# Kernel optimization log

Hardware: AMD Instinct MI355X
Metric: run time of the kernel (lower is better)

## Reference

```python
import jax, jax.numpy as jnp
import numpy as np
from jax import lax

B, D, E, H, W = 256, 64, 16, 64, 64
PROJ, FC, NA = 512, 1024, 2

def _conv(x, w, pad):
    # x: [N,C,H,W], w: [O,I,kh,kw]
    return lax.conv_general_dilated(x, w, (1, 1), [(pad, pad), (pad, pad)],
                                    dimension_numbers=('NCHW', 'OIHW', 'NCHW'))

def _maxpool2(x):
    return lax.reduce_window(x, -jnp.inf, lax.max, (1, 1, 2, 2), (1, 1, 2, 2), 'VALID')

def _sample_conv(x, w, b):
    # per-sample conv with its own gathered expert weights: x [D,h,w], w [D,D,3,3]
    y = lax.conv_general_dilated(x[None], w, (1, 1), [(1, 1), (1, 1)],
                                 dimension_numbers=('NCHW', 'OIHW', 'NCHW'))[0]
    return y + b[:, None, None]

_expert_conv = jax.vmap(_sample_conv)  # batch of samples, each with its own kernel

def setup_inputs() -> dict:
    key = jax.random.key(0)
    ks = jax.random.split(key, 12)
    s = 0.05
    return {
        'image': jax.random.normal(ks[0], (B, 3, H, W), jnp.float32),
        'question': jax.random.randint(ks[1], (B, 8), 0, E),
        'stem_w0': jax.random.normal(ks[2], (D, 3, 3, 3), jnp.float32) * s,
        'stem_b0': jnp.zeros((D,), jnp.float32),
        'stem_w': jax.random.normal(ks[3], (3, D, D, 3, 3), jnp.float32) * s,
        'stem_b': jnp.zeros((3, D), jnp.float32),
        'exp_w1': jax.random.normal(ks[4], (E, D, D, 3, 3), jnp.float32) * s,
        'exp_b1': jnp.zeros((E, D), jnp.float32),
        'exp_w2': jax.random.normal(ks[5], (E, D, D, 3, 3), jnp.float32) * s,
        'exp_b2': jnp.zeros((E, D), jnp.float32),
        'proj_w': jax.random.normal(ks[6], (PROJ, D, 1, 1), jnp.float32) * s,
        'proj_b': jnp.zeros((PROJ,), jnp.float32),
        'fc1_w': jax.random.normal(ks[7], (FC, PROJ * 8 * 8), jnp.float32) * 0.01,
        'fc1_b': jnp.zeros((FC,), jnp.float32),
        'fc2_w': jax.random.normal(ks[8], (NA, FC), jnp.float32) * 0.01,
        'fc2_b': jnp.zeros((NA,), jnp.float32),
    }

def reference(image, question, stem_w0, stem_b0, stem_w, stem_b,
              exp_w1, exp_b1, exp_w2, exp_b2,
              proj_w, proj_b, fc1_w, fc1_b, fc2_w, fc2_b):
    # --- stem: 4 conv3x3 + ReLU, maxpool after layers 0 and 2 (64->32->16) ---
    h = jax.nn.relu(_conv(image, stem_w0, 1) + stem_b0[None, :, None, None])
    h = _maxpool2(h)
    h = jax.nn.relu(_conv(h, stem_w[0], 1) + stem_b[0][None, :, None, None])
    h = jax.nn.relu(_conv(h, stem_w[1], 1) + stem_b[1][None, :, None, None])
    h = _maxpool2(h)
    h = jax.nn.relu(_conv(h, stem_w[2], 1) + stem_b[2][None, :, None, None])
    # --- chain1 routing: cols (lhs=4, rel=5, rhs=7) each pick a ResidualBlock expert ---
    for col in (4, 5, 7):
        idx = question[:, col]                       # [B] expert ids
        w1, b1 = exp_w1[idx], exp_b1[idx]            # gather per-sample kernels
        w2, b2 = exp_w2[idx], exp_b2[idx]
        mid = jax.nn.relu(_expert_conv(h, w1, b1))   # conv1 + ReLU
        out = _expert_conv(mid, w2, b2)              # conv2 (no BN)
        h = jax.nn.relu(h + out)                     # residual + ReLU
    # --- classifier: 1x1 proj + ReLU, maxpool2, flatten, fc, fc ---
    c = jax.nn.relu(_conv(h, proj_w, 0) + proj_b[None, :, None, None])  # [B,512,16,16]
    c = _maxpool2(c)                                                     # [B,512,8,8]
    c = c.reshape(c.shape[0], -1)                                        # [B,32768]
    c = jax.nn.relu(c @ fc1_w.T + fc1_b)
    return c @ fc2_w.T + fc2_b                                           # [B,2]
```

## Files before the change

### kernel.cpp

```cpp
#include <hip/hip_runtime.h>
#include <cstddef>


typedef _Float16 half8 __attribute__((ext_vector_type(8)));
typedef _Float16 half4_t __attribute__((ext_vector_type(4)));
typedef float f32x4 __attribute__((ext_vector_type(4)));

#define LO_SCALE 2048.0f
#define LO_INV (1.0f / 2048.0f)

__global__ void transw_k(const float* __restrict__ src, float* __restrict__ dst,
                         int O, int I, int K, int total) {
    int id = blockIdx.x * 256 + threadIdx.x;
    if (id >= total) return;
    int OIK = O * I * K;
    int n = id / OIK, rem = id % OIK;
    int o = rem / (I * K), r2 = rem % (I * K);
    int i = r2 / K, k = r2 % K;
    dst[(size_t)n * OIK + (i * K + k) * O + o] = src[id];
}

__global__ void wxform_k(const float* __restrict__ src, _Float16* __restrict__ dst,
                         int nlayers) {
    int id = blockIdx.x * 256 + threadIdx.x;
    if (id >= nlayers * 36864) return;
    int layer = id / 36864, idx = id % 36864;
    int j = idx & 7, l = (idx >> 3) & 63, nt = (idx >> 9) & 3;
    int icc = (idx >> 11) & 1, tap = idx >> 12;
    int kl = (l >> 4) * 8 + j, ic = icc * 32 + kl, oc = nt * 16 + (l & 15);
    float v = src[(size_t)layer * 36864 + (oc * 64 + ic) * 9 + tap];
    _Float16 hi = (_Float16)v;
    _Float16 lo = (_Float16)((v - (float)hi) * LO_SCALE);
    dst[(size_t)layer * 73728 + idx] = hi;
    dst[(size_t)layer * 73728 + 36864 + idx] = lo;
}

__global__ __launch_bounds__(256)
void conv1_k(const float* __restrict__ img, const float* __restrict__ w0t,
             const float* __restrict__ b0, float* __restrict__ out) {
    int b = blockIdx.x, tile = blockIdx.y;
    int typ = (tile >> 1) * 16, txp = (tile & 1) * 16;
    int cy0 = typ * 2, cx0 = txp * 2;
    __shared__ float lds[3][34][34];
    const float* imb = img + (size_t)b * 3 * 64 * 64;
    for (int i = threadIdx.x; i < 3 * 34 * 34; i += 256) {
        int c = i / 1156, rem = i % 1156, r = rem / 34, cc = rem % 34;
        int gy = cy0 - 1 + r, gx = cx0 - 1 + cc;
        float v = 0.f;
        if (gy >= 0 && gy < 64 && gx >= 0 && gx < 64) v = imb[(c * 64 + gy) * 64 + gx];
        lds[c][r][cc] = v;
    }
    __syncthreads();
    int pyl = threadIdx.x >> 4, pxl = threadIdx.x & 15;
    float win[3][4][4];
#pragma unroll
    for (int c = 0; c < 3; ++c)
#pragma unroll
        for (int wy = 0; wy < 4; ++wy)
#pragma unroll
            for (int wx = 0; wx < 4; ++wx)
                win[c][wy][wx] = lds[c][2 * pyl + wy][2 * pxl + wx];
    int py = typ + pyl, px = txp + pxl;
    for (int oc = 0; oc < 64; ++oc) {
        float a00 = 0, a01 = 0, a10 = 0, a11 = 0;
#pragma unroll
        for (int c = 0; c < 3; ++c)
#pragma unroll
            for (int ky = 0; ky < 3; ++ky)
#pragma unroll
                for (int kx = 0; kx < 3; ++kx) {
                    float w = w0t[(c * 9 + ky * 3 + kx) * 64 + oc];
                    a00 = fmaf(win[c][0 + ky][0 + kx], w, a00);
                    a01 = fmaf(win[c][0 + ky][1 + kx], w, a01);
                    a10 = fmaf(win[c][1 + ky][0 + kx], w, a10);
                    a11 = fmaf(win[c][1 + ky][1 + kx], w, a11);
                }
        float bv = b0[oc];
        float v = fmaxf(fmaxf(a00 + bv, 0.f), fmaxf(a01 + bv, 0.f));
        v = fmaxf(v, fmaxf(fmaxf(a10 + bv, 0.f), fmaxf(a11 + bv, 0.f)));
        out[(((size_t)b * 32 + py) * 32 + px) * 64 + oc] = v;
    }
}

template <int S, bool POOL, bool RES>
__global__ __launch_bounds__(256, 2)
void convm_k(const float* __restrict__ in, float* __restrict__ out,
             const _Float16* __restrict__ wf, const float* __restrict__ bias,
             const float* __restrict__ res, const int* __restrict__ question,
             int qcol) {
    int b = blockIdx.x, t = blockIdx.y;
    constexpr int NTX = S / 16;
    int ty0 = (t / NTX) * 8, tx0 = (t % NTX) * 16;

    __shared__ __align__(16) _Float16 lds[2 * 7200];

    int tid = threadIdx.x, lane = tid & 63, wv = tid >> 6;
    const _Float16* wb = wf;
    const float* bb = bias;
    if (question) {
        int idx = question[b * 8 + qcol];
        wb += (size_t)idx * 73728;
        bb += idx * 64;
    }
    float bv[4];
#pragma unroll
    for (int nt = 0; nt < 4; ++nt) bv[nt] = bb[nt * 16 + (lane & 15)];

    f32x4 acc1[2][4] = {};
    f32x4 acc2[2][4] = {};

    int am = lane & 15;
    int k0 = (lane >> 4) * 8;

    for (int icc = 0; icc < 2; ++icc) {
        __syncthreads();
        for (int i = tid; i < 1440; i += 256) {
            int pix = i >> 3, j4 = i & 7;
            int hy = pix / 18, hx = pix % 18;
            int gy = ty0 + hy - 1, gx = tx0 + hx - 1;
            float4 v = {0.f, 0.f, 0.f, 0.f};
            if (gy >= 0 && gy < S && gx >= 0 && gx < S)
                v = *(const float4*)&in[(((size_t)b * S + gy) * S + gx) * 64 + icc * 32 + j4 * 4];
            _Float16 h0 = (_Float16)v.x, h1 = (_Float16)v.y;
            _Float16 h2 = (_Float16)v.z, h3 = (_Float16)v.w;
            half4_t hh = {h0, h1, h2, h3};
            half4_t ll = {(_Float16)((v.x - (float)h0) * LO_SCALE),
                          (_Float16)((v.y - (float)h1) * LO_SCALE),
                          (_Float16)((v.z - (float)h2) * LO_SCALE),
                          (_Float16)((v.w - (float)h3) * LO_SCALE)};
            *(half4_t*)&lds[pix * 40 + j4 * 4] = hh;
            *(half4_t*)&lds[7200 + pix * 40 + j4 * 4] = ll;
        }
        __syncthreads();

#pragma unroll
        for (int ky = 0; ky < 3; ++ky)
#pragma unroll
            for (int kx = 0; kx < 3; ++kx) {
                int tap = ky * 3 + kx;
                const _Float16* wp = wb + (tap * 2 + icc) * 2048 + lane * 8;
                half8 bhi[4], blo[4];
#pragma unroll
                for (int nt = 0; nt < 4; ++nt) {
                    bhi[nt] = *(const half8*)(wp + nt * 512);
                    blo[nt] = *(const half8*)(wp + nt * 512 + 36864);
                }
#pragma unroll
                for (int mt = 0; mt < 2; ++mt) {
                    int MT = wv * 2 + mt;
                    int Q = MT * 4 + (am >> 2), s = am & 3;
                    int py = (Q >> 3) * 2 + (s >> 1), px = (Q & 7) * 2 + (s & 1);
                    const _Float16* ap = &lds[((py + ky) * 18 + (px + kx)) * 40 + k0];
                    half8 ahi = *(const half8*)ap;
                    half8 alo = *(const half8*)(ap + 7200);
#pragma unroll
                    for (int nt = 0; nt < 4; ++nt) {
                        acc1[mt][nt] = __builtin_amdgcn_mfma_f32_16x16x32_f16(
                            ahi, bhi[nt], acc1[mt][nt], 0, 0, 0);
                        acc2[mt][nt] = __builtin_amdgcn_mfma_f32_16x16x32_f16(
                            ahi, blo[nt], acc2[mt][nt], 0, 0, 0);
                        acc2[mt][nt] = __builtin_amdgcn_mfma_f32_16x16x32_f16(
                            alo, bhi[nt], acc2[mt][nt], 0, 0, 0);
                    }
                }
            }
    }

    int cn = lane & 15, rq = lane >> 4;
#pragma unroll
    for (int mt = 0; mt < 2; ++mt) {
        int MT = wv * 2 + mt;
        int Q = MT * 4 + rq;
        int qy = Q >> 3, qx = Q & 7;
#pragma unroll
        for (int nt = 0; nt < 4; ++nt) {
            int oc = nt * 16 + cn;
            float vals[4];
#pragma unroll
            for (int r = 0; r < 4; ++r)
                vals[r] = acc1[mt][nt][r] + acc2[mt][nt][r] * LO_INV + bv[nt];
            if (POOL) {
                float m = fmaxf(fmaxf(vals[0], vals[1]), fmaxf(vals[2], vals[3]));
                m = fmaxf(m, 0.f);
                int opy = (ty0 >> 1) + qy, opx = (tx0 >> 1) + qx;
                out[(((size_t)b * (S / 2) + opy) * (S / 2) + opx) * 64 + oc] = m;
            } else {
#pragma unroll
                for (int r = 0; r < 4; ++r) {
                    int py = qy * 2 + (r >> 1), px = qx * 2 + (r & 1);
                    size_t o = (((size_t)b * S + (ty0 + py)) * S + (tx0 + px)) * 64 + oc;
                    float v = vals[r];
                    if (RES) v += res[o];
                    out[o] = fmaxf(v, 0.f);
                }
            }
        }
    }
}

__global__ __launch_bounds__(256)
void proj_k(const float* __restrict__ in, const float* __restrict__ wt ,
            const float* __restrict__ bias, float* __restrict__ out) {
    int b = blockIdx.x;
    __shared__ float lds[16384];
    const float* inb = in + (size_t)b * 16384;
    for (int i = threadIdx.x; i < 16384; i += 256) lds[i] = inb[i];
    __syncthreads();
    int lane = threadIdx.x & 63, wv = threadIdx.x >> 6;
    int oc = (blockIdx.y * 4 + wv) * 64 + lane;
    float w[64];
#pragma unroll
    for (int ic = 0; ic < 64; ++ic) w[ic] = wt[ic * 512 + oc];
    float bvv = bias[oc];
    for (int pp = 0; pp < 64; ++pp) {
        int ppy = pp >> 3, ppx = pp & 7;
        float m = 0.f;
#pragma unroll
        for (int d = 0; d < 4; ++d) {
            int py = ppy * 2 + (d >> 1), px = ppx * 2 + (d & 1);
            const float* ap = &lds[(py * 16 + px) * 64];
            float acc = bvv;
#pragma unroll
            for (int ic = 0; ic < 64; ++ic) acc = fmaf(ap[ic], w[ic], acc);
            m = fmaxf(m, acc);
        }
        out[(size_t)b * 32768 + (size_t)oc * 64 + pp] = m;
    }
}

__global__ __launch_bounds__(256)
void fc1m_k(const float* __restrict__ A, const float* __restrict__ W,
            float* __restrict__ partial ) {
    int bid = blockIdx.x;
    int lid = (bid & 7) * 64 + (bid >> 3);
    int mt = lid & 1, nt = (lid >> 1) & 7, ks = lid >> 4;
    int m0 = mt * 128, n0 = nt * 128;
    const float* Ab = A + (size_t)m0 * 32768 + ks * 1024;
    const float* Wb = W + (size_t)n0 * 32768 + ks * 1024;

    __shared__ __align__(16) _Float16 lds[20480];
    _Float16* sa = lds;
    _Float16* sb = lds + 10240;

    int tid = threadIdx.x, lane = tid & 63, wv = tid >> 6;
    int wm = (wv & 1) * 64, wn = (wv >> 1) * 64;

    f32x4 acc1[4][4] = {};
    f32x4 acc2[4][4] = {};

    int row[4], c4[4];
#pragma unroll
    for (int p = 0; p < 4; ++p) {
        int idx = p * 256 + tid;
        row[p] = idx >> 3;
        c4[p] = (idx & 7) << 2;
    }

    float4 ra[4], rw[4];
#pragma unroll
    for (int p = 0; p < 4; ++p) {
        ra[p] = *(const float4*)&Ab[(size_t)row[p] * 32768 + c4[p]];
        rw[p] = *(const float4*)&Wb[(size_t)row[p] * 32768 + c4[p]];
    }

    for (int kt = 0; kt < 32; ++kt) {
#pragma unroll
        for (int p = 0; p < 4; ++p) {
            float4 v = ra[p];
            _Float16 h0 = (_Float16)v.x, h1 = (_Float16)v.y;
            _Float16 h2 = (_Float16)v.z, h3 = (_Float16)v.w;
            half4_t hh = {h0, h1, h2, h3};
            half4_t ll = {(_Float16)((v.x - (float)h0) * LO_SCALE),
                          (_Float16)((v.y - (float)h1) * LO_SCALE),
                          (_Float16)((v.z - (float)h2) * LO_SCALE),
                          (_Float16)((v.w - (float)h3) * LO_SCALE)};
            *(half4_t*)&sa[row[p] * 40 + c4[p]] = hh;
            *(half4_t*)&sa[5120 + row[p] * 40 + c4[p]] = ll;
            float4 u = rw[p];
            _Float16 g0 = (_Float16)u.x, g1 = (_Float16)u.y;
            _Float16 g2 = (_Float16)u.z, g3 = (_Float16)u.w;
            half4_t gh = {g0, g1, g2, g3};
            half4_t gl = {(_Float16)((u.x - (float)g0) * LO_SCALE),
                          (_Float16)((u.y - (float)g1) * LO_SCALE),
                          (_Float16)((u.z - (float)g2) * LO_SCALE),
                          (_Float16)((u.w - (float)g3) * LO_SCALE)};
            *(half4_t*)&sb[row[p] * 40 + c4[p]] = gh;
            *(half4_t*)&sb[5120 + row[p] * 40 + c4[p]] = gl;
        }
        __syncthreads();
        if (kt < 31) {
            int kb = (kt + 1) * 32;
#pragma unroll
            for (int p = 0; p < 4; ++p) {
                ra[p] = *(const float4*)&Ab[(size_t)row[p] * 32768 + kb + c4[p]];
                rw[p] = *(const float4*)&Wb[(size_t)row[p] * 32768 + kb + c4[p]];
            }
        }
        int koff = (lane >> 4) * 8;
        int fr = lane & 15;
        half8 bh[4], bl[4];
#pragma unroll
        for (int nf = 0; nf < 4; ++nf) {
            int r = wn + nf * 16 + fr;
            bh[nf] = *(const half8*)&sb[r * 40 + koff];
            bl[nf] = *(const half8*)&sb[5120 + r * 40 + koff];
        }
#pragma unroll
        for (int mf = 0; mf < 4; ++mf) {
            int r = wm + mf * 16 + fr;
            half8 ah = *(const half8*)&sa[r * 40 + koff];
            half8 al = *(const half8*)&sa[5120 + r * 40 + koff];
#pragma unroll
            for (int nf = 0; nf < 4; ++nf) {
                acc1[mf][nf] = __builtin_amdgcn_mfma_f32_16x16x32_f16(
                    ah, bh[nf], acc1[mf][nf], 0, 0, 0);
                acc2[mf][nf] = __builtin_amdgcn_mfma_f32_16x16x32_f16(
                    ah, bl[nf], acc2[mf][nf], 0, 0, 0);
                acc2[mf][nf] = __builtin_amdgcn_mfma_f32_16x16x32_f16(
                    al, bh[nf], acc2[mf][nf], 0, 0, 0);
            }
        }
        __syncthreads();
    }

    int rq = lane >> 4, cn = lane & 15;
    float* pb = partial + (size_t)ks * 262144;
#pragma unroll
    for (int mf = 0; mf < 4; ++mf)
#pragma unroll
        for (int nf = 0; nf < 4; ++nf) {
            int n = n0 + wn + nf * 16 + cn;
#pragma unroll
            for (int r = 0; r < 4; ++r) {
                int m = m0 + wm + mf * 16 + rq * 4 + r;
                pb[(size_t)m * 1024 + n] = acc1[mf][nf][r] + acc2[mf][nf][r] * LO_INV;
            }
        }
}

__global__ __launch_bounds__(256)
void fc1red_k(const float* __restrict__ partial, const float* __restrict__ b1,
              float* __restrict__ fc1o_t ) {
    int m = blockIdx.x;
    int n0 = threadIdx.x * 4;
    float4 s = {0.f, 0.f, 0.f, 0.f};
    for (int ks = 0; ks < 32; ++ks) {
        float4 v = *(const float4*)&partial[((size_t)ks * 256 + m) * 1024 + n0];
        s.x += v.x; s.y += v.y; s.z += v.z; s.w += v.w;
    }
    fc1o_t[(size_t)(n0 + 0) * 256 + m] = fmaxf(s.x + b1[n0 + 0], 0.f);
    fc1o_t[(size_t)(n0 + 1) * 256 + m] = fmaxf(s.y + b1[n0 + 1], 0.f);
    fc1o_t[(size_t)(n0 + 2) * 256 + m] = fmaxf(s.z + b1[n0 + 2], 0.f);
    fc1o_t[(size_t)(n0 + 3) * 256 + m] = fmaxf(s.w + b1[n0 + 3], 0.f);
}

__global__ __launch_bounds__(256)
void fc2a_k(const float* __restrict__ a_t, const float* __restrict__ W2,
            float* __restrict__ p2) {
    int n2 = blockIdx.x, ks = blockIdx.y;
    int m = threadIdx.x;
    float acc = 0.f;
    for (int k = ks * 256; k < ks * 256 + 256; ++k)
        acc = fmaf(a_t[(size_t)k * 256 + m], W2[n2 * 1024 + k], acc);
    p2[((size_t)n2 * 4 + ks) * 256 + m] = acc;
}

__global__ __launch_bounds__(512)
void fc2b_k(const float* __restrict__ p2, const float* __restrict__ b2,
            float* __restrict__ out) {
    int i = threadIdx.x;
    int m = i >> 1, n2 = i & 1;
    float s = b2[n2];
#pragma unroll
    for (int ks = 0; ks < 4; ++ks) s += p2[((size_t)n2 * 4 + ks) * 256 + m];
    out[m * 2 + n2] = s;
}

extern "C" void kernel_launch(void* const* d_in, const int* in_sizes, int n_in,
                              void* d_out, int out_size, void* d_ws, size_t ws_size,
                              hipStream_t stream) {
    const float* image   = (const float*)d_in[0];
    const int*   question= (const int*)d_in[1];
    const float* stem_w0 = (const float*)d_in[2];
    const float* stem_b0 = (const float*)d_in[3];
    const float* stem_w  = (const float*)d_in[4];
    const float* stem_b  = (const float*)d_in[5];
    const float* exp_w1  = (const float*)d_in[6];
    const float* exp_b1  = (const float*)d_in[7];
    const float* exp_w2  = (const float*)d_in[8];
    const float* exp_b2  = (const float*)d_in[9];
    const float* proj_w  = (const float*)d_in[10];
    const float* proj_b  = (const float*)d_in[11];
    const float* fc1_w   = (const float*)d_in[12];
    const float* fc1_b   = (const float*)d_in[13];
    const float* fc2_w   = (const float*)d_in[14];
    const float* fc2_b   = (const float*)d_in[15];
    (void)in_sizes; (void)n_in; (void)out_size; (void)ws_size;

    float* ws = (float*)d_ws;
    const size_t A = 16777216, P2N = 4194304;
    float* p1    = ws;
    float* h2    = ws + A;
    float* p2    = ws + 2 * A;
    float* wtr   = ws + 2 * A + P2N;
    float* w0t   = wtr;
    float* projt = wtr + 1728;
    float* pfc2  = wtr + 1728 + 32768;
    _Float16* f16b = (_Float16*)(wtr + 36544);
    _Float16* stemtF = f16b;
    _Float16* e1tF   = f16b + 3 * 73728;
    _Float16* e2tF   = e1tF + 16 * 73728;
    float* hA    = ws;
    float* hB    = ws + P2N;
    float* hC    = ws + 2 * P2N;
    float* pool3 = h2;
    float* fc1o  = h2 + 8388608;
    float* fc1p  = ws;

    transw_k<<<(1728 + 255) / 256, 256, 0, stream>>>(stem_w0, w0t, 64, 3, 9, 1728);
    transw_k<<<(32768 + 255) / 256, 256, 0, stream>>>(proj_w, projt, 512, 64, 1, 32768);
    wxform_k<<<(3 * 36864 + 255) / 256, 256, 0, stream>>>(stem_w, stemtF, 3);
    wxform_k<<<(16 * 36864 + 255) / 256, 256, 0, stream>>>(exp_w1, e1tF, 16);
    wxform_k<<<(16 * 36864 + 255) / 256, 256, 0, stream>>>(exp_w2, e2tF, 16);

    conv1_k<<<dim3(256, 4), 256, 0, stream>>>(image, w0t, stem_b0, p1);
    convm_k<32, false, false><<<dim3(256, 8), 256, 0, stream>>>(
        p1, h2, stemtF, stem_b, nullptr, nullptr, 0);
    convm_k<32, true, false><<<dim3(256, 8), 256, 0, stream>>>(
        h2, p2, stemtF + 73728, stem_b + 64, nullptr, nullptr, 0);
    convm_k<16, false, false><<<dim3(256, 2), 256, 0, stream>>>(
        p2, hA, stemtF + 2 * 73728, stem_b + 128, nullptr, nullptr, 0);

    const int cols[3] = {4, 5, 7};
    float* hin = hA;
    float* hmid = hB;
    float* hout = hC;
    for (int r = 0; r < 3; ++r) {
        convm_k<16, false, false><<<dim3(256, 2), 256, 0, stream>>>(
            hin, hmid, e1tF, exp_b1, nullptr, question, cols[r]);
        convm_k<16, false, true><<<dim3(256, 2), 256, 0, stream>>>(
            hmid, hout, e2tF, exp_b2, hin, question, cols[r]);
        float* tp = hin; hin = hout; hout = hmid; hmid = tp;
    }

    proj_k<<<dim3(256, 2), 256, 0, stream>>>(hin, projt, proj_b, pool3);
    fc1m_k<<<512, 256, 0, stream>>>(pool3, fc1_w, fc1p);
    fc1red_k<<<256, 256, 0, stream>>>(fc1p, fc1_b, fc1o);
    fc2a_k<<<dim3(2, 4), 256, 0, stream>>>(fc1o, fc2_w, pfc2);
    fc2b_k<<<1, 512, 0, stream>>>(pfc2, fc2_b, (float*)d_out);
}
```

Measured before the change: 514.4 us.

## Move 1x1 projection to split-fp16 MFMA and stage conv1 stores through LDS

The scalar FP32 1x1 projection with fused maxpool is rewritten as an MFMA GEMM. It uses hi/lo fp16 splitting (three MFMAs per tile) to keep roughly fp32 accuracy, and the weights are pre-packed into the MFMA fragment layout by a new transform kernel. Pooled results are transposed through LDS so global writes are coalesced. Separately, conv1 now buffers 16 output channels per pass in LDS and writes them out coalesced instead of issuing strided per-channel stores. The cost is extra conversion work and synchronisation in both kernels.

Measured after the change: 626.9 us. 1.22x slower.

```diff
diff --git a/kernel.cpp b/kernel.cpp
--- a/kernel.cpp
+++ b/kernel.cpp
@@ -35,6 +35,18 @@
     dst[(size_t)layer * 73728 + 36864 + idx] = lo;
 }
 
+__global__ void pwxform_k(const float* __restrict__ src, _Float16* __restrict__ dst) {
+    int id = blockIdx.x * 256 + threadIdx.x;
+    if (id >= 32768) return;
+    int j = id & 7, l = (id >> 3) & 63, icc = (id >> 9) & 1, nt = id >> 10;
+    int kl = (l >> 4) * 8 + j, ic = icc * 32 + kl, oc = nt * 16 + (l & 15);
+    float v = src[oc * 64 + ic];
+    _Float16 hi = (_Float16)v;
+    _Float16 lo = (_Float16)((v - (float)hi) * LO_SCALE);
+    dst[id] = hi;
+    dst[32768 + id] = lo;
+}
+
 __global__ __launch_bounds__(256)
 void conv1_k(const float* __restrict__ img, const float* __restrict__ w0t,
              const float* __restrict__ b0, float* __restrict__ out) {
@@ -42,6 +54,7 @@
     int typ = (tile >> 1) * 16, txp = (tile & 1) * 16;
     int cy0 = typ * 2, cx0 = txp * 2;
     __shared__ float lds[3][34][34];
+    __shared__ float lo[256 * 17];
     const float* imb = img + (size_t)b * 3 * 64 * 64;
     for (int i = threadIdx.x; i < 3 * 34 * 34; i += 256) {
         int c = i / 1156, rem = i % 1156, r = rem / 34, cc = rem % 34;
@@ -60,25 +73,37 @@
 #pragma unroll
             for (int wx = 0; wx < 4; ++wx)
                 win[c][wy][wx] = lds[c][2 * pyl + wy][2 * pxl + wx];
-    int py = typ + pyl, px = txp + pxl;
-    for (int oc = 0; oc < 64; ++oc) {
-        float a00 = 0, a01 = 0, a10 = 0, a11 = 0;
-#pragma unroll
-        for (int c = 0; c < 3; ++c)
-#pragma unroll
-            for (int ky = 0; ky < 3; ++ky)
-#pragma unroll
-                for (int kx = 0; kx < 3; ++kx) {
-                    float w = w0t[(c * 9 + ky * 3 + kx) * 64 + oc];
-                    a00 = fmaf(win[c][0 + ky][0 + kx], w, a00);
-                    a01 = fmaf(win[c][0 + ky][1 + kx], w, a01);
-                    a10 = fmaf(win[c][1 + ky][0 + kx], w, a10);
-                    a11 = fmaf(win[c][1 + ky][1 + kx], w, a11);
-                }
-        float bv = b0[oc];
-        float v = fmaxf(fmaxf(a00 + bv, 0.f), fmaxf(a01 + bv, 0.f));
-        v = fmaxf(v, fmaxf(fmaxf(a10 + bv, 0.f), fmaxf(a11 + bv, 0.f)));
-        out[(((size_t)b * 32 + py) * 32 + px) * 64 + oc] = v;
+    for (int ch = 0; ch < 4; ++ch) {
+        __syncthreads();
+#pragma unroll
+        for (int j = 0; j < 16; ++j) {
+            int oc = ch * 16 + j;
+            float a00 = 0, a01 = 0, a10 = 0, a11 = 0;
+#pragma unroll
+            for (int c = 0; c < 3; ++c)
+#pragma unroll
+                for (int ky = 0; ky < 3; ++ky)
+#pragma unroll
+                    for (int kx = 0; kx < 3; ++kx) {
+                        float w = w0t[(c * 9 + ky * 3 + kx) * 64 + oc];
+                        a00 = fmaf(win[c][0 + ky][0 + kx], w, a00);
+                        a01 = fmaf(win[c][0 + ky][1 + kx], w, a01);
+                        a10 = fmaf(win[c][1 + ky][0 + kx], w, a10);
+                        a11 = fmaf(win[c][1 + ky][1 + kx], w, a11);
+                    }
+            float bv = b0[oc];
+            float v = fmaxf(fmaxf(a00 + bv, 0.f), fmaxf(a01 + bv, 0.f));
+            v = fmaxf(v, fmaxf(fmaxf(a10 + bv, 0.f), fmaxf(a11 + bv, 0.f)));
+            lo[threadIdx.x * 17 + j] = v;
+        }
+        __syncthreads();
+#pragma unroll
+        for (int r = 0; r < 16; ++r) {
+            int f = r * 256 + threadIdx.x;
+            int pl = f >> 4, j = f & 15;
+            int py = typ + (pl >> 4), px = txp + (pl & 15);
+            out[(((size_t)b * 32 + py) * 32 + px) * 64 + ch * 16 + j] = lo[pl * 17 + j];
+        }
     }
 }
 
@@ -199,32 +224,90 @@
 }
 
 __global__ __launch_bounds__(256)
-void proj_k(const float* __restrict__ in, const float* __restrict__ wt ,
-            const float* __restrict__ bias, float* __restrict__ out) {
+void projm_k(const float* __restrict__ in ,
+             const _Float16* __restrict__ pw, const float* __restrict__ bias,
+             float* __restrict__ out ) {
     int b = blockIdx.x;
-    __shared__ float lds[16384];
-    const float* inb = in + (size_t)b * 16384;
-    for (int i = threadIdx.x; i < 16384; i += 256) lds[i] = inb[i];
-    __syncthreads();
-    int lane = threadIdx.x & 63, wv = threadIdx.x >> 6;
-    int oc = (blockIdx.y * 4 + wv) * 64 + lane;
-    float w[64];
-#pragma unroll
-    for (int ic = 0; ic < 64; ++ic) w[ic] = wt[ic * 512 + oc];
-    float bvv = bias[oc];
-    for (int pp = 0; pp < 64; ++pp) {
-        int ppy = pp >> 3, ppx = pp & 7;
-        float m = 0.f;
-#pragma unroll
-        for (int d = 0; d < 4; ++d) {
-            int py = ppy * 2 + (d >> 1), px = ppx * 2 + (d & 1);
-            const float* ap = &lds[(py * 16 + px) * 64];
-            float acc = bvv;
-#pragma unroll
-            for (int ic = 0; ic < 64; ++ic) acc = fmaf(ap[ic], w[ic], acc);
-            m = fmaxf(m, acc);
-        }
-        out[(size_t)b * 32768 + (size_t)oc * 64 + pp] = m;
+    __shared__ float lt[64 * 65];
+    int tid = threadIdx.x, lane = tid & 63, wv = tid >> 6;
+    int row = lane & 15, cseg = lane >> 4;
+
+    half8 ah[4][2], al[4][2];
+#pragma unroll
+    for (int mt = 0; mt < 4; ++mt) {
+        int MT = wv * 4 + mt;
+        int Q = MT * 4 + (row >> 2), s = row & 3;
+        int y = (Q >> 3) * 2 + (s >> 1), x = (Q & 7) * 2 + (s & 1);
+        const float* ip = in + ((size_t)b * 256 + y * 16 + x) * 64 + cseg * 8;
+#pragma unroll
+        for (int icc = 0; icc < 2; ++icc) {
+            float4 v0 = *(const float4*)(ip + icc * 32);
+            float4 v1 = *(const float4*)(ip + icc * 32 + 4);
+            _Float16 h0 = (_Float16)v0.x, h1 = (_Float16)v0.y;
+            _Float16 h2 = (_Float16)v0.z, h3 = (_Float16)v0.w;
+            _Float16 h4 = (_Float16)v1.x, h5 = (_Float16)v1.y;
+            _Float16 h6 = (_Float16)v1.z, h7 = (_Float16)v1.w;
+            ah[mt][icc] = (half8){h0, h1, h2, h3, h4, h5, h6, h7};
+            al[mt][icc] = (half8){(_Float16)((v0.x - (float)h0) * LO_SCALE),
+                                  (_Float16)((v0.y - (float)h1) * LO_SCALE),
+                                  (_Float16)((v0.z - (float)h2) * LO_SCALE),
+                                  (_Float16)((v0.w - (float)h3) * LO_SCALE),
+                                  (_Float16)((v1.x - (float)h4) * LO_SCALE),
+                                  (_Float16)((v1.y - (float)h5) * LO_SCALE),
+                                  (_Float16)((v1.z - (float)h6) * LO_SCALE),
+                                  (_Float16)((v1.w - (float)h7) * LO_SCALE)};
+        }
+    }
+
+    for (int ogl = 0; ogl < 4; ++ogl) {
+        int og = blockIdx.y * 4 + ogl;
+        half8 bh[4][2], bl[4][2];
+#pragma unroll
+        for (int ntl = 0; ntl < 4; ++ntl)
+#pragma unroll
+            for (int icc = 0; icc < 2; ++icc) {
+                int nt = og * 4 + ntl;
+                const _Float16* wp = pw + ((nt * 2 + icc) * 64 + lane) * 8;
+                bh[ntl][icc] = *(const half8*)wp;
+                bl[ntl][icc] = *(const half8*)(wp + 32768);
+            }
+        f32x4 a1[4][4] = {};
+        f32x4 a2[4][4] = {};
+#pragma unroll
+        for (int icc = 0; icc < 2; ++icc)
+#pragma unroll
+            for (int mt = 0; mt < 4; ++mt)
+#pragma unroll
+                for (int ntl = 0; ntl < 4; ++ntl) {
+                    a1[mt][ntl] = __builtin_amdgcn_mfma_f32_16x16x32_f16(
+                        ah[mt][icc], bh[ntl][icc], a1[mt][ntl], 0, 0, 0);
+                    a2[mt][ntl] = __builtin_amdgcn_mfma_f32_16x16x32_f16(
+                        ah[mt][icc], bl[ntl][icc], a2[mt][ntl], 0, 0, 0);
+                    a2[mt][ntl] = __builtin_amdgcn_mfma_f32_16x16x32_f16(
+                        al[mt][icc], bh[ntl][icc], a2[mt][ntl], 0, 0, 0);
+                }
+        if (ogl) __syncthreads();
+#pragma unroll
+        for (int mt = 0; mt < 4; ++mt) {
+            int Qg = (wv * 4 + mt) * 4 + (lane >> 4);
+#pragma unroll
+            for (int ntl = 0; ntl < 4; ++ntl) {
+                float bvv = bias[og * 64 + ntl * 16 + (lane & 15)];
+                float v0 = a1[mt][ntl][0] + a2[mt][ntl][0] * LO_INV + bvv;
+                float v1 = a1[mt][ntl][1] + a2[mt][ntl][1] * LO_INV + bvv;
+                float v2 = a1[mt][ntl][2] + a2[mt][ntl][2] * LO_INV + bvv;
+                float v3 = a1[mt][ntl][3] + a2[mt][ntl][3] * LO_INV + bvv;
+                float m = fmaxf(fmaxf(fmaxf(v0, v1), fmaxf(v2, v3)), 0.f);
+                lt[(ntl * 16 + (lane & 15)) * 65 + Qg] = m;
+            }
+        }
+        __syncthreads();
+#pragma unroll
+        for (int r = 0; r < 16; ++r) {
+            int f = r * 256 + tid;
+            int ol = f >> 6, q = f & 63;
+            out[(size_t)b * 32768 + og * 4096 + ol * 64 + q] = lt[ol * 65 + q];
+        }
     }
 }
 
@@ -404,7 +487,7 @@
     float* p2    = ws + 2 * A;
     float* wtr   = ws + 2 * A + P2N;
     float* w0t   = wtr;
-    float* projt = wtr + 1728;
+    _Float16* pwF = (_Float16*)(wtr + 1728);
     float* pfc2  = wtr + 1728 + 32768;
     _Float16* f16b = (_Float16*)(wtr + 36544);
     _Float16* stemtF = f16b;
@@ -418,7 +501,7 @@
     float* fc1p  = ws;
 
     transw_k<<<(1728 + 255) / 256, 256, 0, stream>>>(stem_w0, w0t, 64, 3, 9, 1728);
-    transw_k<<<(32768 + 255) / 256, 256, 0, stream>>>(proj_w, projt, 512, 64, 1, 32768);
+    pwxform_k<<<128, 256, 0, stream>>>(proj_w, pwF);
     wxform_k<<<(3 * 36864 + 255) / 256, 256, 0, stream>>>(stem_w, stemtF, 3);
     wxform_k<<<(16 * 36864 + 255) / 256, 256, 0, stream>>>(exp_w1, e1tF, 16);
     wxform_k<<<(16 * 36864 + 255) / 256, 256, 0, stream>>>(exp_w2, e2tF, 16);
@@ -443,7 +526,7 @@
         float* tp = hin; hin = hout; hout = hmid; hmid = tp;
     }
 
-    proj_k<<<dim3(256, 2), 256, 0, stream>>>(hin, projt, proj_b, pool3);
+    projm_k<<<dim3(256, 2), 256, 0, stream>>>(hin, pwF, proj_b, pool3);
     fc1m_k<<<512, 256, 0, stream>>>(pool3, fc1_w, fc1p);
     fc1red_k<<<256, 256, 0, stream>>>(fc1p, fc1_b, fc1o);
     fc2a_k<<<dim3(2, 4), 256, 0, stream>>>(fc1o, fc2_w, pfc2);
```
